# Optimization experiments

Measured on AMD Instinct MI355X. Metric: run time of the kernel, lower is better.

Reference implementation:

```python
import jax, jax.numpy as jnp
import numpy as np

DIM = 1536
HEADS = 12
HD = DIM // HEADS  # 128
EPS = 1e-6
SINK_SIZE = 1          # frames
MAX_ATTN = 1920        # tokens (sliding window)


def setup_inputs() -> dict:
    key = jax.random.key(0)
    ks = jax.random.split(key, 10)
    B = 1
    F, H, W = 8, 16, 24
    L = F * H * W  # 3072
    s = 0.02
    inp = {
        "x": jax.random.normal(ks[0], (B, L, DIM), jnp.float32),
        "seq_lens": jnp.array([L], jnp.int32),
        "grid_sizes": jnp.array([[F, H, W]], jnp.int32),
        "freqs": jax.random.normal(ks[1], (1024, HD // 2, 2), jnp.float32),
        "wq": jax.random.normal(ks[2], (DIM, DIM), jnp.float32) * s,
        "bq": jnp.zeros((DIM,), jnp.float32),
        "wk": jax.random.normal(ks[3], (DIM, DIM), jnp.float32) * s,
        "bk": jnp.zeros((DIM,), jnp.float32),
        "wv": jax.random.normal(ks[4], (DIM, DIM), jnp.float32) * s,
        "bv": jnp.zeros((DIM,), jnp.float32),
        "wo": jax.random.normal(ks[5], (DIM, DIM), jnp.float32) * s,
        "bo": jnp.zeros((DIM,), jnp.float32),
        "nq_w": jnp.ones((DIM,), jnp.float32),
        "nk_w": jnp.ones((DIM,), jnp.float32),
    }
    return inp


def _rmsnorm(x, w):
    # WanRMSNorm: x * rsqrt(mean(x^2) + eps) * weight
    return x * jax.lax.rsqrt(jnp.mean(x * x, axis=-1, keepdims=True) + EPS) * w


def _rope(x, F, H, W, fc):
    # x: [B, L, n, d]; fc: complex [1024, d//2]
    B, L, n, d = x.shape
    c = d // 2
    c1 = c - 2 * (c // 3)  # temporal split
    c2 = c // 3
    f0, f1, f2 = fc[:, :c1], fc[:, c1:c1 + c2], fc[:, c1 + c2:]
    fr = jnp.concatenate([
        jnp.broadcast_to(f0[:F, None, None, :], (F, H, W, c1)),
        jnp.broadcast_to(f1[None, :H, None, :], (F, H, W, c2)),
        jnp.broadcast_to(f2[None, None, :W, :], (F, H, W, c2)),
    ], axis=-1).reshape(L, 1, c)  # [L, 1, c]
    xp = x.reshape(B, L, n, c, 2)
    xc = jax.lax.complex(xp[..., 0], xp[..., 1])  # [B, L, n, c]
    xr = xc * fr[None]
    return jnp.stack([jnp.real(xr), jnp.imag(xr)], axis=-1).reshape(B, L, n, d)


def reference(x, seq_lens, grid_sizes, freqs, wq, bq, wk, bk, wv, bv, wo, bo, nq_w, nk_w):
    B, L, _ = x.shape
    gs = np.asarray(grid_sizes)[0]
    F, H, W = int(gs[0]), int(gs[1]), int(gs[2])
    fs = H * W  # frame_seqlen
    sink = SINK_SIZE * fs

    q = _rmsnorm(x @ wq.T + bq, nq_w).reshape(B, L, HEADS, HD)
    k = _rmsnorm(x @ wk.T + bk, nk_w).reshape(B, L, HEADS, HD)
    v = (x @ wv.T + bv).reshape(B, L, HEADS, HD)

    fc = jax.lax.complex(freqs[..., 0], freqs[..., 1])  # [1024, HD//2]
    q = _rope(q, F, H, W, fc)
    k = _rope(k, F, H, W, fc)

    # sink + windowed frame-causal block mask (flex_attention block_mask)
    idx = jnp.arange(L)
    qf = idx // fs
    kf = idx // fs
    mask = (kf[None, :] <= qf[:, None]) & (
        (idx[None, :] < sink) | (idx[None, :] >= (qf[:, None] + 1) * fs - MAX_ATTN)
    )  # [L, L]

    scale = 1.0 / np.float32(np.sqrt(HD))
    scores = jnp.einsum('bqnd,bknd->bnqk', q, k) * scale
    scores = jnp.where(mask[None, None], scores, jnp.float32(-1e30))
    attn = jax.nn.softmax(scores, axis=-1)
    out = jnp.einsum('bnqk,bknd->bqnd', attn, v).reshape(B, L, DIM)
    return out @ wo.T + bo
```

## Files before the change

### kernel.cpp

```cpp
#include <hip/hip_runtime.h>
#include <stdint.h>

#define DIMC 1536
#define LTOK 3072
#define HEADS 12
#define HD 128
#define FS 384
#define MAXATTN 1920
#define HTOK 1152
#define NHT 1920

typedef __attribute__((ext_vector_type(4))) float f32x4;
typedef __attribute__((ext_vector_type(8))) short bf16x8;
typedef __attribute__((ext_vector_type(4))) unsigned int u32x4;

__device__ __forceinline__ unsigned short f2bf(float f) {
  union { float f; unsigned int u; } c; c.f = f;
  unsigned int u = c.u + 0x7fffu + ((c.u >> 16) & 1u);
  return (unsigned short)(u >> 16);
}
__device__ __forceinline__ float bf2f(unsigned short s) {
  union { unsigned int u; float f; } c; c.u = (unsigned int)s << 16; return c.f;
}

__device__ __forceinline__ void dma16(const void* g, void* l) {
  __builtin_amdgcn_global_load_lds(
      (const __attribute__((address_space(1))) unsigned int*)g,
      (__attribute__((address_space(3))) unsigned int*)l, 16, 0, 0);
}

__global__ __launch_bounds__(256)
void cvt_all_k(const float* __restrict__ x, const float* __restrict__ wq,
               const float* __restrict__ wk, const float* __restrict__ wv,
               const float* __restrict__ wo,
               unsigned short* __restrict__ xb, unsigned short* __restrict__ wqb,
               unsigned short* __restrict__ wkb, unsigned short* __restrict__ wvb,
               unsigned short* __restrict__ wob)
{
  const int i = blockIdx.x * 256 + threadIdx.x;
  const int n0 = LTOK * DIMC / 4;
  const int nw = DIMC * DIMC / 4;
  const float* src; unsigned short* dst; int off;
  if (i < n0) { src = x; dst = xb; off = i; }
  else {
    int j = i - n0; int w = j / nw; off = j - w * nw;
    src = (w == 0) ? wq : (w == 1) ? wk : (w == 2) ? wv : wo;
    dst = (w == 0) ? wqb : (w == 1) ? wkb : (w == 2) ? wvb : wob;
  }
  float4 f = ((const float4*)src)[off];
  uint2 o;
  o.x = (unsigned int)f2bf(f.x) | ((unsigned int)f2bf(f.y) << 16);
  o.y = (unsigned int)f2bf(f.z) | ((unsigned int)f2bf(f.w) << 16);
  ((uint2*)dst)[off] = o;
}

#define GBUF (128 * 32)
__global__ __launch_bounds__(256)
void gemm_qkv(const unsigned short* __restrict__ A,
              const unsigned short* __restrict__ B0,
              const unsigned short* __restrict__ B1,
              const unsigned short* __restrict__ B2,
              const float* __restrict__ bias0,
              const float* __restrict__ bias1,
              const float* __restrict__ bias2,
              unsigned short* __restrict__ o0, unsigned short* __restrict__ o1,
              unsigned short* __restrict__ o2)
{
  const int z = blockIdx.z;
  const unsigned short* Bw = (z == 0) ? B0 : (z == 1) ? B1 : B2;
  const float* bias = (z == 0) ? bias0 : (z == 1) ? bias1 : bias2;
  unsigned short* outp = (z == 0) ? o0 : (z == 1) ? o1 : o2;

  __shared__ __align__(16) unsigned short lA[2 * GBUF];
  __shared__ __align__(16) unsigned short lB[2 * GBUF];

  const int tid = threadIdx.x;
  const int wave = tid >> 6;
  const int lane = tid & 63;
  const int m0 = blockIdx.y * 128;
  const int n0 = blockIdx.x * 128;
  const int wm = (wave >> 1) * 64;
  const int wn = (wave & 1) * 64;

  f32x4 acc[4][4] = {};

  const int srow = tid >> 2;
  const int scol = (tid & 3) * 8;
  const int fr = lane & 15;
  const int fk = (lane >> 4) * 8;

  unsigned short* laS = lA + srow * 32 + scol;
  unsigned short* lbS = lB + srow * 32 + scol;
  const unsigned short* ga0 = A  + (size_t)(m0 + srow)      * DIMC + scol;
  const unsigned short* ga1 = A  + (size_t)(m0 + srow + 64) * DIMC + scol;
  const unsigned short* gb0 = Bw + (size_t)(n0 + srow)      * DIMC + scol;
  const unsigned short* gb1 = Bw + (size_t)(n0 + srow + 64) * DIMC + scol;

  dma16(ga0, laS);
  dma16(ga1, laS + 64 * 32);
  dma16(gb0, lbS);
  dma16(gb1, lbS + 64 * 32);

  for (int t = 0; t < 48; ++t) {
    const int cur = (t & 1) * GBUF;
    __syncthreads();
    if (t < 47) {
      const int nxt = GBUF - cur;
      const int k0n = (t + 1) * 32;
      dma16(ga0 + k0n, laS + nxt);
      dma16(ga1 + k0n, laS + nxt + 64 * 32);
      dma16(gb0 + k0n, lbS + nxt);
      dma16(gb1 + k0n, lbS + nxt + 64 * 32);
    }

    bf16x8 af[4], bf[4];
#pragma unroll
    for (int i = 0; i < 4; ++i)
      af[i] = *(const bf16x8*)&lA[cur + (wm + i * 16 + fr) * 32 + fk];
#pragma unroll
    for (int j = 0; j < 4; ++j)
      bf[j] = *(const bf16x8*)&lB[cur + (wn + j * 16 + fr) * 32 + fk];
#pragma unroll
    for (int i = 0; i < 4; ++i)
#pragma unroll
      for (int j = 0; j < 4; ++j)
        acc[i][j] = __builtin_amdgcn_mfma_f32_16x16x32_bf16(af[i], bf[j], acc[i][j], 0, 0, 0);
  }

  const int col = lane & 15;
  const int rb = (lane >> 4) * 4;
#pragma unroll
  for (int j = 0; j < 4; ++j) {
    const int gn = n0 + wn + j * 16 + col;
    const float bv = bias[gn];
#pragma unroll
    for (int i = 0; i < 4; ++i)
#pragma unroll
      for (int r = 0; r < 4; ++r) {
        const int gm = m0 + wm + i * 16 + rb + r;
        outp[(size_t)gm * DIMC + gn] = f2bf(acc[i][j][r] + bv);
      }
  }
}

__global__ __launch_bounds__(512)
void gemm_wo(const unsigned short* __restrict__ A,
             const unsigned short* __restrict__ Bw,
             const float* __restrict__ bias,
             float* __restrict__ outp)
{
  __shared__ __align__(16) unsigned short lA[2 * GBUF];
  __shared__ __align__(16) unsigned short lB[2 * GBUF];

  const int tid = threadIdx.x;
  const int wave = tid >> 6;
  const int lane = tid & 63;
  const int m0 = blockIdx.y * 128;
  const int n0 = blockIdx.x * 128;
  const int wm = (wave >> 1) * 32;
  const int wn = (wave & 1) * 64;

  f32x4 acc[2][4] = {};

  const int srow = tid >> 2;
  const int scol = (tid & 3) * 8;
  const int fr = lane & 15;
  const int fk = (lane >> 4) * 8;

  unsigned short* laS = lA + srow * 32 + scol;
  unsigned short* lbS = lB + srow * 32 + scol;
  const unsigned short* ga = A  + (size_t)(m0 + srow) * DIMC + scol;
  const unsigned short* gb = Bw + (size_t)(n0 + srow) * DIMC + scol;

  dma16(ga, laS);
  dma16(gb, lbS);

  for (int t = 0; t < 48; ++t) {
    const int cur = (t & 1) * GBUF;
    __syncthreads();
    if (t < 47) {
      const int nxt = GBUF - cur;
      const int k0n = (t + 1) * 32;
      dma16(ga + k0n, laS + nxt);
      dma16(gb + k0n, lbS + nxt);
    }

    bf16x8 af[2], bf[4];
#pragma unroll
    for (int i = 0; i < 2; ++i)
      af[i] = *(const bf16x8*)&lA[cur + (wm + i * 16 + fr) * 32 + fk];
#pragma unroll
    for (int j = 0; j < 4; ++j)
      bf[j] = *(const bf16x8*)&lB[cur + (wn + j * 16 + fr) * 32 + fk];
#pragma unroll
    for (int i = 0; i < 2; ++i)
#pragma unroll
      for (int j = 0; j < 4; ++j)
        acc[i][j] = __builtin_amdgcn_mfma_f32_16x16x32_bf16(af[i], bf[j], acc[i][j], 0, 0, 0);
  }

  const int col = lane & 15;
  const int rb = (lane >> 4) * 4;
#pragma unroll
  for (int j = 0; j < 4; ++j) {
    const int gn = n0 + wn + j * 16 + col;
    const float bv = bias[gn];
#pragma unroll
    for (int i = 0; i < 2; ++i)
#pragma unroll
      for (int r = 0; r < 4; ++r) {
        const int gm = m0 + wm + i * 16 + rb + r;
        outp[(size_t)gm * DIMC + gn] = acc[i][j][r] + bv;
      }
  }
}

__device__ __forceinline__ int vperm4(int G) {
  return (((G >> 3) & 1) << 3) | (((G >> 1) & 1) << 2) | ((G & 1) << 1) | ((G >> 2) & 1);
}

__global__ __launch_bounds__(256)
void post_qkv_k(unsigned short* __restrict__ q, unsigned short* __restrict__ k,
                const unsigned short* __restrict__ v, unsigned short* __restrict__ vt,
                const float* __restrict__ nqw, const float* __restrict__ nkw,
                const float* __restrict__ freqs)
{
  const int bx = blockIdx.x;
  const int tid = threadIdx.x;
  if (bx < 2 * LTOK) {
    const int which = bx >= LTOK;
    const int tok = bx - which * LTOK;
    unsigned short* row = (which ? k : q) + (size_t)tok * DIMC;
    const float* nw = which ? nkw : nqw;
    const float sc = which ? 1.f : (0.08838834764831845f * 1.4426950408889634f);
    const int base = tid * 6;

    float vv[6];
    float ss = 0.f;
#pragma unroll
    for (int j = 0; j < 6; ++j) {
      vv[j] = bf2f(row[base + j]);
      ss += vv[j] * vv[j];
    }
#pragma unroll
    for (int off = 1; off < 64; off <<= 1) ss += __shfl_xor(ss, off);
    __shared__ float wsum[4];
    if ((tid & 63) == 0) wsum[tid >> 6] = ss;
    __syncthreads();
    const float total = wsum[0] + wsum[1] + wsum[2] + wsum[3];
    const float rms = rsqrtf(total * (1.f / DIMC) + 1e-6f);

    const int f = tok / FS;
    const int rem = tok - f * FS;
    const int h = rem / 24;
    const int w = rem - h * 24;

#pragma unroll
    for (int pp = 0; pp < 3; ++pp) {
      const int P = (base >> 1) + pp;
      const int p = P & 63;
      const int t = (p < 22) ? f : ((p < 43) ? h : w);
      const float fre = freqs[t * 128 + p * 2];
      const float fim = freqs[t * 128 + p * 2 + 1];
      const float e = vv[2 * pp]     * rms * nw[base + 2 * pp];
      const float o = vv[2 * pp + 1] * rms * nw[base + 2 * pp + 1];
      row[base + 2 * pp]     = f2bf((e * fre - o * fim) * sc);
      row[base + 2 * pp + 1] = f2bf((e * fim + o * fre) * sc);
    }
  } else {
    const int c0 = bx - 2 * LTOK;
    const int tb = (c0 % 48) * 64;
    const int db = (c0 / 48) * 64;
    __shared__ __align__(16) unsigned short t[64 * 72];
#pragma unroll
    for (int it = 0; it < 2; ++it) {
      int c = tid + it * 256;
      int tok = c >> 3, dc = (c & 7) * 8;
      uint4 val = *(const uint4*)(v + (size_t)(tb + tok) * DIMC + db + dc);
      unsigned short tmp[8];
      *(uint4*)tmp = val;
#pragma unroll
      for (int j = 0; j < 8; ++j) t[(dc + j) * 72 + tok] = tmp[j];
    }
    __syncthreads();
#pragma unroll
    for (int it = 0; it < 4; ++it) {
      int c = tid + it * 256;
      int d = c >> 4, G = c & 15;
      *(uint2*)(vt + ((size_t)db + d) * LTOK + tb + vperm4(G) * 4) =
          *(const uint2*)&t[d * 72 + G * 4];
    }
  }
}

#define KBUF (64 * 128)
#define VBUF (128 * 64)
__global__ __launch_bounds__(256, 2)
void attn_flash(const unsigned short* __restrict__ q,
                const unsigned short* __restrict__ k,
                const unsigned short* __restrict__ vt,
                unsigned short* __restrict__ ab,
                float* __restrict__ Opart,
                float* __restrict__ mlbuf)
{
  const int bid = blockIdx.x;
  int qb, head, chunk, nchunks;
  if (bid < 360) { const int hb = bid >> 1; qb = 23 - hb / 12; head = hb % 12; chunk = bid & 1; nchunks = 2; }
  else           { const int lb = bid - 360; qb = 8 - lb / 12; head = lb % 12; chunk = 0; nchunks = 1; }

  const int q0 = qb * 128;
  const int qf = qb / 3;
  const int kend = (qf + 1) * FS;
  const int s2 = kend - MAXATTN;
  const bool two = (s2 > FS);
  const int nt1 = (two ? FS : kend) >> 6;
  const int nt  = nt1 + (two ? (MAXATTN >> 6) : 0);
  const int half = nt / nchunks;
  const int tstart = chunk * half, tend = tstart + half;

  const int tid = threadIdx.x;
  const int wave = tid >> 6, lane = tid & 63;
  const int col = lane & 15;
  const int g = lane >> 4;
  const int g4 = g * 4;

  __shared__ __align__(16) unsigned short Kl[2 * KBUF];
  __shared__ __align__(16) unsigned short Vtl[2 * VBUF];

  bf16x8 qfA[4], qfB[4];
  {
    const unsigned short* qr0 = q + (size_t)(q0 + wave * 32 + col) * DIMC + head * HD;
#pragma unroll
    for (int kk = 0; kk < 4; ++kk) {
      qfA[kk] = *(const bf16x8*)(qr0 + kk * 32 + g * 8);
      qfB[kk] = *(const bf16x8*)(qr0 + (size_t)16 * DIMC + kk * 32 + g * 8);
    }
  }

  f32x4 o0[8] = {}, o1[8] = {};
  float m0 = -3.0e38f, l0 = 0.f, m1 = -3.0e38f, l1 = 0.f;

  const int krow = tid >> 4;
  const int kc8  = ((tid & 15) ^ krow) * 8;
  const unsigned short* kg = k + (size_t)krow * DIMC + head * HD + kc8;
  const int vrow = tid >> 3;
  const int vc8  = ((tid & 7) ^ (vrow & 7)) * 8;
  const unsigned short* vg = vt + ((size_t)head * HD + vrow) * LTOK + vc8;
  unsigned short* kl = Kl + tid * 8;
  unsigned short* vl = Vtl + tid * 8;

  {
    const int kb = (tstart < nt1) ? tstart * 64 : s2 + (tstart - nt1) * 64;
    const unsigned short* kp = kg + (size_t)kb * DIMC;
    dma16(kp,                     kl);
    dma16(kp + (size_t)16 * DIMC, kl + 16 * 128);
    dma16(kp + (size_t)32 * DIMC, kl + 32 * 128);
    dma16(kp + (size_t)48 * DIMC, kl + 48 * 128);
    const unsigned short* vp = vg + kb;
    dma16(vp,                     vl);
    dma16(vp + (size_t)32 * LTOK, vl + 32 * 64);
    dma16(vp + (size_t)64 * LTOK, vl + 64 * 64);
    dma16(vp + (size_t)96 * LTOK, vl + 96 * 64);
  }

  for (int t = tstart; t < tend; ++t) {
    const int kcur = ((t - tstart) & 1) * KBUF;
    const int vcur = ((t - tstart) & 1) * VBUF;
    __syncthreads();

    if (t + 1 < tend) {
      const int kb = (t + 1 < nt1) ? (t + 1) * 64 : s2 + (t + 1 - nt1) * 64;
      const int knxt = KBUF - kcur, vnxt = VBUF - vcur;
      const unsigned short* kp = kg + (size_t)kb * DIMC;
      dma16(kp,                     kl + knxt);
      dma16(kp + (size_t)16 * DIMC, kl + knxt + 16 * 128);
      dma16(kp + (size_t)32 * DIMC, kl + knxt + 32 * 128);
      dma16(kp + (size_t)48 * DIMC, kl + knxt + 48 * 128);
      const unsigned short* vp = vg + kb;
      dma16(vp,                     vl + vnxt);
      dma16(vp + (size_t)32 * LTOK, vl + vnxt + 32 * 64);
      dma16(vp + (size_t)64 * LTOK, vl + vnxt + 64 * 64);
      dma16(vp + (size_t)96 * LTOK, vl + vnxt + 96 * 64);
    }

    f32x4 sA[4] = {}, sB[4] = {};
#pragma unroll
    for (int kt = 0; kt < 4; ++kt) {
      const unsigned short* kr = &Kl[kcur + (kt * 16 + col) * 128];
#pragma unroll
      for (int kk = 0; kk < 4; ++kk) {
        bf16x8 kfr = *(const bf16x8*)(kr + ((kk * 4 + g) ^ col) * 8);
        sA[kt] = __builtin_amdgcn_mfma_f32_16x16x32_bf16(kfr, qfA[kk], sA[kt], 0, 0, 0);
        sB[kt] = __builtin_amdgcn_mfma_f32_16x16x32_bf16(kfr, qfB[kk], sB[kt], 0, 0, 0);
      }
    }

    unsigned int A0, A1, A2, A3, A4, A5, A6, A7;
    float alA;
    {
      float mx = sA[0][0];
#pragma unroll
      for (int kt = 0; kt < 4; ++kt)
#pragma unroll
        for (int r = 0; r < 4; ++r) mx = fmaxf(mx, sA[kt][r]);
      mx = fmaxf(mx, __shfl_xor(mx, 16));
      mx = fmaxf(mx, __shfl_xor(mx, 32));
      const float mn = fmaxf(m0, mx);
      alA = exp2f(m0 - mn);
      m0 = mn;
      float rs = 0.f;
#define PKA(KT, PA, PB)                                        \
      {                                                        \
        const unsigned short p0 = f2bf(exp2f(sA[KT][0] - mn)); \
        const unsigned short p1 = f2bf(exp2f(sA[KT][1] - mn)); \
        const unsigned short p2 = f2bf(exp2f(sA[KT][2] - mn)); \
        const unsigned short p3 = f2bf(exp2f(sA[KT][3] - mn)); \
        rs += bf2f(p0) + bf2f(p1) + bf2f(p2) + bf2f(p3);       \
        PA = (unsigned int)p0 | ((unsigned int)p1 << 16);      \
        PB = (unsigned int)p2 | ((unsigned int)p3 << 16);      \
      }
      PKA(0, A0, A1) PKA(1, A2, A3) PKA(2, A4, A5) PKA(3, A6, A7)
#undef PKA
      rs += __shfl_xor(rs, 16);
      rs += __shfl_xor(rs, 32);
      l0 = l0 * alA + rs;
    }
    unsigned int B0, B1, B2, B3, B4, B5, B6, B7;
    float alB;
    {
      float mx = sB[0][0];
#pragma unroll
      for (int kt = 0; kt < 4; ++kt)
#pragma unroll
        for (int r = 0; r < 4; ++r) mx = fmaxf(mx, sB[kt][r]);
      mx = fmaxf(mx, __shfl_xor(mx, 16));
      mx = fmaxf(mx, __shfl_xor(mx, 32));
      const float mn = fmaxf(m1, mx);
      alB = exp2f(m1 - mn);
      m1 = mn;
      float rs = 0.f;
#define PKB(KT, PA, PB)                                        \
      {                                                        \
        const unsigned short p0 = f2bf(exp2f(sB[KT][0] - mn)); \
        const unsigned short p1 = f2bf(exp2f(sB[KT][1] - mn)); \
        const unsigned short p2 = f2bf(exp2f(sB[KT][2] - mn)); \
        const unsigned short p3 = f2bf(exp2f(sB[KT][3] - mn)); \
        rs += bf2f(p0) + bf2f(p1) + bf2f(p2) + bf2f(p3);       \
        PA = (unsigned int)p0 | ((unsigned int)p1 << 16);      \
        PB = (unsigned int)p2 | ((unsigned int)p3 << 16);      \
      }
      PKB(0, B0, B1) PKB(1, B2, B3) PKB(2, B4, B5) PKB(3, B6, B7)
#undef PKB
      rs += __shfl_xor(rs, 16);
      rs += __shfl_xor(rs, 32);
      l1 = l1 * alB + rs;
    }

#pragma unroll
    for (int dt = 0; dt < 8; ++dt) { o0[dt] *= alA; o1[dt] *= alB; }

    u32x4 tA0, tA1, tB0, tB1;
    tA0[0] = A0; tA0[1] = A1; tA0[2] = A2; tA0[3] = A3;
    tA1[0] = A4; tA1[1] = A5; tA1[2] = A6; tA1[3] = A7;
    tB0[0] = B0; tB0[1] = B1; tB0[2] = B2; tB0[3] = B3;
    tB1[0] = B4; tB1[1] = B5; tB1[2] = B6; tB1[3] = B7;
    const bf16x8 pfA0 = __builtin_bit_cast(bf16x8, tA0);
    const bf16x8 pfA1 = __builtin_bit_cast(bf16x8, tA1);
    const bf16x8 pfB0 = __builtin_bit_cast(bf16x8, tB0);
    const bf16x8 pfB1 = __builtin_bit_cast(bf16x8, tB1);

    const int vx0 = (g ^ (col & 7)) * 8;
    const int vx1 = ((4 + g) ^ (col & 7)) * 8;
#pragma unroll
    for (int dt = 0; dt < 8; ++dt) {
      const unsigned short* vr = &Vtl[vcur + (dt * 16 + col) * 64];
      bf16x8 vf0 = *(const bf16x8*)(vr + vx0);
      o0[dt] = __builtin_amdgcn_mfma_f32_16x16x32_bf16(vf0, pfA0, o0[dt], 0, 0, 0);
      o1[dt] = __builtin_amdgcn_mfma_f32_16x16x32_bf16(vf0, pfB0, o1[dt], 0, 0, 0);
      bf16x8 vf1 = *(const bf16x8*)(vr + vx1);
      o0[dt] = __builtin_amdgcn_mfma_f32_16x16x32_bf16(vf1, pfA1, o0[dt], 0, 0, 0);
      o1[dt] = __builtin_amdgcn_mfma_f32_16x16x32_bf16(vf1, pfB1, o1[dt], 0, 0, 0);
    }
  }

  const int qrow0 = q0 + wave * 32 + col;
  if (nchunks == 1) {
    const float i0 = 1.f / l0, i1 = 1.f / l1;
    unsigned short* or0 = ab + (size_t)qrow0 * DIMC + head * HD;
    unsigned short* or1 = or0 + (size_t)16 * DIMC;
#pragma unroll
    for (int dt = 0; dt < 8; ++dt) {
      uint2 pk;
      pk.x = (unsigned int)f2bf(o0[dt][0] * i0) | ((unsigned int)f2bf(o0[dt][1] * i0) << 16);
      pk.y = (unsigned int)f2bf(o0[dt][2] * i0) | ((unsigned int)f2bf(o0[dt][3] * i0) << 16);
      *(uint2*)(or0 + dt * 16 + g4) = pk;
      pk.x = (unsigned int)f2bf(o1[dt][0] * i1) | ((unsigned int)f2bf(o1[dt][1] * i1) << 16);
      pk.y = (unsigned int)f2bf(o1[dt][2] * i1) | ((unsigned int)f2bf(o1[dt][3] * i1) << 16);
      *(uint2*)(or1 + dt * 16 + g4) = pk;
    }
  } else {
    const int tokp0 = qrow0 - HTOK;
    float* ob0 = Opart + ((size_t)(chunk * NHT + tokp0) * HEADS + head) * HD;
    float* ob1 = Opart + ((size_t)(chunk * NHT + tokp0 + 16) * HEADS + head) * HD;
#pragma unroll
    for (int dt = 0; dt < 8; ++dt) {
      *(f32x4*)(ob0 + dt * 16 + g4) = o0[dt];
      *(f32x4*)(ob1 + dt * 16 + g4) = o1[dt];
    }
    if (lane < 16) {
      float* mlp0 = mlbuf + 2 * ((size_t)(chunk * NHT + tokp0) * HEADS + head);
      float* mlp1 = mlbuf + 2 * ((size_t)(chunk * NHT + tokp0 + 16) * HEADS + head);
      mlp0[0] = m0; mlp0[1] = l0;
      mlp1[0] = m1; mlp1[1] = l1;
    }
  }
}

__global__ __launch_bounds__(384)
void merge_k(const float* __restrict__ Opart, const float* __restrict__ mlbuf,
             unsigned short* __restrict__ ab)
{
  const int tokp = blockIdx.x;
  const int tid = threadIdx.x;
  const int e = tid * 4;
  const int head = e >> 7;
  const size_t r0 = (size_t)tokp * DIMC + e;
  float4 o0 = *(const float4*)(Opart + r0);
  float4 o1 = *(const float4*)(Opart + (size_t)NHT * DIMC + r0);
  const float* ml0 = mlbuf + 2 * ((size_t)tokp * HEADS + head);
  const float* ml1 = mlbuf + 2 * ((size_t)(NHT + tokp) * HEADS + head);
  const float m0 = ml0[0], l0 = ml0[1], m1 = ml1[0], l1 = ml1[1];
  const float mm = fmaxf(m0, m1);
  const float a0 = exp2f(m0 - mm), a1 = exp2f(m1 - mm);
  const float inv = 1.f / (l0 * a0 + l1 * a1);
  uint2 pk;
  pk.x = (unsigned int)f2bf((o0.x * a0 + o1.x * a1) * inv) |
         ((unsigned int)f2bf((o0.y * a0 + o1.y * a1) * inv) << 16);
  pk.y = (unsigned int)f2bf((o0.z * a0 + o1.z * a1) * inv) |
         ((unsigned int)f2bf((o0.w * a0 + o1.w * a1) * inv) << 16);
  *(uint2*)(ab + (size_t)(HTOK + tokp) * DIMC + e) = pk;
}

extern "C" void kernel_launch(void* const* d_in, const int* in_sizes, int n_in,
                              void* d_out, int out_size, void* d_ws, size_t ws_size,
                              hipStream_t stream)
{
  (void)in_sizes; (void)n_in; (void)out_size; (void)ws_size;
  const float* x     = (const float*)d_in[0];
  const float* freqs = (const float*)d_in[3];
  const float* wq    = (const float*)d_in[4];
  const float* bq    = (const float*)d_in[5];
  const float* wk    = (const float*)d_in[6];
  const float* bk    = (const float*)d_in[7];
  const float* wv    = (const float*)d_in[8];
  const float* bv    = (const float*)d_in[9];
  const float* wo    = (const float*)d_in[10];
  const float* bo    = (const float*)d_in[11];
  const float* nqw   = (const float*)d_in[12];
  const float* nkw   = (const float*)d_in[13];

  char* ws = (char*)d_ws;
  size_t off = 0;
  auto take = [&](size_t bytes) -> void* {
    void* p = ws + off; off += (bytes + 255) & ~(size_t)255; return p;
  };
  unsigned short* wob = (unsigned short*)take((size_t)DIMC * DIMC * 2);
  unsigned short* qb  = (unsigned short*)take((size_t)LTOK * DIMC * 2);
  unsigned short* kb  = (unsigned short*)take((size_t)LTOK * DIMC * 2);
  unsigned short* vb  = (unsigned short*)take((size_t)LTOK * DIMC * 2);
  unsigned short* ab  = (unsigned short*)take((size_t)LTOK * DIMC * 2);
  unsigned short* vtb = (unsigned short*)take((size_t)LTOK * DIMC * 2);
  unsigned short* xb  = (unsigned short*)take((size_t)LTOK * DIMC * 2);
  unsigned short* wqb = (unsigned short*)take((size_t)DIMC * DIMC * 2);
  unsigned short* wkb = (unsigned short*)take((size_t)DIMC * DIMC * 2);
  unsigned short* wvb = (unsigned short*)take((size_t)DIMC * DIMC * 2);
  float* mlb = (float*)take((size_t)2 * NHT * HEADS * 2 * sizeof(float));
  float* Opart = (float*)xb;

  cvt_all_k<<<dim3(13824), dim3(256), 0, stream>>>(x, wq, wk, wv, wo,
                                                   xb, wqb, wkb, wvb, wob);

  gemm_qkv<<<dim3(DIMC / 128, LTOK / 128, 3), dim3(256), 0, stream>>>(
      xb, wqb, wkb, wvb, bq, bk, bv, qb, kb, vb);

  post_qkv_k<<<dim3(2 * LTOK + 1152), dim3(256), 0, stream>>>(
      qb, kb, vb, vtb, nqw, nkw, freqs);

  attn_flash<<<dim3(468), dim3(256), 0, stream>>>(qb, kb, vtb, ab, Opart, mlb);
  merge_k<<<dim3(NHT), dim3(384), 0, stream>>>(Opart, mlb, ab);

  gemm_wo<<<dim3(DIMC / 128, LTOK / 128), dim3(512), 0, stream>>>(
      ab, wob, bo, (float*)d_out);
}
```

Baseline: 318.5 us.

## Fuse V transpose into QKV GEMM epilogue and retile GEMMs with swizzled K=64 LDS

The QKV GEMM now writes V directly in the transposed, permuted layout the attention kernel reads, which removes the separate transpose blocks from post_qkv_k and one round trip of V through memory. Both GEMMs move from double-buffered K=32 stages to single-buffered K=64 stages with an XOR-swizzled LDS layout meant to reduce bank conflicts. gemm_wo also changes from 512-thread 128x128 tiles to 256-thread 64x128 tiles. Dropping double buffering means global loads are no longer overlapped with MFMA work, which could expose load latency, and the transposed V stores are 8-byte scattered writes.

```diff
diff --git a/kernel.cpp b/kernel.cpp
--- a/kernel.cpp
+++ b/kernel.cpp
@@ -27,6 +27,10 @@
   __builtin_amdgcn_global_load_lds(
       (const __attribute__((address_space(1))) unsigned int*)g,
       (__attribute__((address_space(3))) unsigned int*)l, 16, 0, 0);
+}
+
+__device__ __forceinline__ int vperm4(int G) {
+  return (((G >> 3) & 1) << 3) | (((G >> 1) & 1) << 2) | ((G & 1) << 1) | ((G >> 2) & 1);
 }
 
 __global__ __launch_bounds__(256)
@@ -54,7 +58,6 @@
   ((uint2*)dst)[off] = o;
 }
 
-#define GBUF (128 * 32)
 __global__ __launch_bounds__(256)
 void gemm_qkv(const unsigned short* __restrict__ A,
               const unsigned short* __restrict__ B0,
@@ -64,15 +67,14 @@
               const float* __restrict__ bias1,
               const float* __restrict__ bias2,
               unsigned short* __restrict__ o0, unsigned short* __restrict__ o1,
-              unsigned short* __restrict__ o2)
+              unsigned short* __restrict__ vt)
 {
   const int z = blockIdx.z;
   const unsigned short* Bw = (z == 0) ? B0 : (z == 1) ? B1 : B2;
   const float* bias = (z == 0) ? bias0 : (z == 1) ? bias1 : bias2;
-  unsigned short* outp = (z == 0) ? o0 : (z == 1) ? o1 : o2;
-
-  __shared__ __align__(16) unsigned short lA[2 * GBUF];
-  __shared__ __align__(16) unsigned short lB[2 * GBUF];
+
+  __shared__ __align__(16) unsigned short lA[128 * 64];
+  __shared__ __align__(16) unsigned short lB[128 * 64];
 
   const int tid = threadIdx.x;
   const int wave = tid >> 6;
@@ -84,119 +86,140 @@
 
   f32x4 acc[4][4] = {};
 
-  const int srow = tid >> 2;
-  const int scol = (tid & 3) * 8;
+  const int srow = tid >> 3;
+  const int scol = ((tid & 7) ^ (srow & 7)) * 8;
+  const unsigned short* ga = A  + (size_t)(m0 + srow) * DIMC + scol;
+  const unsigned short* gb = Bw + (size_t)(n0 + srow) * DIMC + scol;
+  unsigned short* la = lA + tid * 8;
+  unsigned short* lb = lB + tid * 8;
+
   const int fr = lane & 15;
-  const int fk = (lane >> 4) * 8;
-
-  unsigned short* laS = lA + srow * 32 + scol;
-  unsigned short* lbS = lB + srow * 32 + scol;
-  const unsigned short* ga0 = A  + (size_t)(m0 + srow)      * DIMC + scol;
-  const unsigned short* ga1 = A  + (size_t)(m0 + srow + 64) * DIMC + scol;
-  const unsigned short* gb0 = Bw + (size_t)(n0 + srow)      * DIMC + scol;
-  const unsigned short* gb1 = Bw + (size_t)(n0 + srow + 64) * DIMC + scol;
-
-  dma16(ga0, laS);
-  dma16(ga1, laS + 64 * 32);
-  dma16(gb0, lbS);
-  dma16(gb1, lbS + 64 * 32);
-
-  for (int t = 0; t < 48; ++t) {
-    const int cur = (t & 1) * GBUF;
+  const int g = lane >> 4;
+  const int fx = fr & 7;
+
+  for (int k0 = 0; k0 < DIMC; k0 += 64) {
+    dma16(ga + k0,                     la);
+    dma16(ga + k0 + (size_t)32 * DIMC, la + 2048);
+    dma16(ga + k0 + (size_t)64 * DIMC, la + 4096);
+    dma16(ga + k0 + (size_t)96 * DIMC, la + 6144);
+    dma16(gb + k0,                     lb);
+    dma16(gb + k0 + (size_t)32 * DIMC, lb + 2048);
+    dma16(gb + k0 + (size_t)64 * DIMC, lb + 4096);
+    dma16(gb + k0 + (size_t)96 * DIMC, lb + 6144);
     __syncthreads();
-    if (t < 47) {
-      const int nxt = GBUF - cur;
-      const int k0n = (t + 1) * 32;
-      dma16(ga0 + k0n, laS + nxt);
-      dma16(ga1 + k0n, laS + nxt + 64 * 32);
-      dma16(gb0 + k0n, lbS + nxt);
-      dma16(gb1 + k0n, lbS + nxt + 64 * 32);
-    }
-
-    bf16x8 af[4], bf[4];
-#pragma unroll
-    for (int i = 0; i < 4; ++i)
-      af[i] = *(const bf16x8*)&lA[cur + (wm + i * 16 + fr) * 32 + fk];
-#pragma unroll
-    for (int j = 0; j < 4; ++j)
-      bf[j] = *(const bf16x8*)&lB[cur + (wn + j * 16 + fr) * 32 + fk];
-#pragma unroll
-    for (int i = 0; i < 4; ++i)
+
+#pragma unroll
+    for (int kk = 0; kk < 2; ++kk) {
+      const int cx = ((kk * 4 + g) ^ fx) * 8;
+      bf16x8 af[4], bf[4];
+#pragma unroll
+      for (int i = 0; i < 4; ++i)
+        af[i] = *(const bf16x8*)&lA[(wm + i * 16 + fr) * 64 + cx];
 #pragma unroll
       for (int j = 0; j < 4; ++j)
-        acc[i][j] = __builtin_amdgcn_mfma_f32_16x16x32_bf16(af[i], bf[j], acc[i][j], 0, 0, 0);
+        bf[j] = *(const bf16x8*)&lB[(wn + j * 16 + fr) * 64 + cx];
+#pragma unroll
+      for (int i = 0; i < 4; ++i)
+#pragma unroll
+        for (int j = 0; j < 4; ++j)
+          acc[i][j] = __builtin_amdgcn_mfma_f32_16x16x32_bf16(af[i], bf[j], acc[i][j], 0, 0, 0);
+    }
+    __syncthreads();
   }
 
   const int col = lane & 15;
   const int rb = (lane >> 4) * 4;
-#pragma unroll
-  for (int j = 0; j < 4; ++j) {
-    const int gn = n0 + wn + j * 16 + col;
-    const float bv = bias[gn];
-#pragma unroll
-    for (int i = 0; i < 4; ++i)
-#pragma unroll
-      for (int r = 0; r < 4; ++r) {
-        const int gm = m0 + wm + i * 16 + rb + r;
-        outp[(size_t)gm * DIMC + gn] = f2bf(acc[i][j][r] + bv);
+  if (z < 2) {
+    unsigned short* outp = z ? o1 : o0;
+#pragma unroll
+    for (int j = 0; j < 4; ++j) {
+      const int gn = n0 + wn + j * 16 + col;
+      const float bv = bias[gn];
+#pragma unroll
+      for (int i = 0; i < 4; ++i)
+#pragma unroll
+        for (int r = 0; r < 4; ++r) {
+          const int gm = m0 + wm + i * 16 + rb + r;
+          outp[(size_t)gm * DIMC + gn] = f2bf(acc[i][j][r] + bv);
+        }
+    }
+  } else {
+#pragma unroll
+    for (int j = 0; j < 4; ++j) {
+      const int gn = n0 + wn + j * 16 + col;
+      const float bv = bias[gn];
+#pragma unroll
+      for (int i = 0; i < 4; ++i) {
+        const int base = wm + i * 16 + rb;
+        const int tile = base & ~63;
+        const int toka = m0 + tile + vperm4((base & 63) >> 2) * 4;
+        uint2 pk;
+        pk.x = (unsigned int)f2bf(acc[i][j][0] + bv) |
+               ((unsigned int)f2bf(acc[i][j][1] + bv) << 16);
+        pk.y = (unsigned int)f2bf(acc[i][j][2] + bv) |
+               ((unsigned int)f2bf(acc[i][j][3] + bv) << 16);
+        *(uint2*)(vt + (size_t)gn * LTOK + toka) = pk;
       }
-  }
-}
-
-__global__ __launch_bounds__(512)
+    }
+  }
+}
+
+__global__ __launch_bounds__(256)
 void gemm_wo(const unsigned short* __restrict__ A,
              const unsigned short* __restrict__ Bw,
              const float* __restrict__ bias,
              float* __restrict__ outp)
 {
-  __shared__ __align__(16) unsigned short lA[2 * GBUF];
-  __shared__ __align__(16) unsigned short lB[2 * GBUF];
+  __shared__ __align__(16) unsigned short lA[64 * 64];
+  __shared__ __align__(16) unsigned short lB[128 * 64];
 
   const int tid = threadIdx.x;
   const int wave = tid >> 6;
   const int lane = tid & 63;
-  const int m0 = blockIdx.y * 128;
+  const int m0 = blockIdx.y * 64;
   const int n0 = blockIdx.x * 128;
   const int wm = (wave >> 1) * 32;
   const int wn = (wave & 1) * 64;
 
   f32x4 acc[2][4] = {};
 
-  const int srow = tid >> 2;
-  const int scol = (tid & 3) * 8;
-  const int fr = lane & 15;
-  const int fk = (lane >> 4) * 8;
-
-  unsigned short* laS = lA + srow * 32 + scol;
-  unsigned short* lbS = lB + srow * 32 + scol;
+  const int srow = tid >> 3;
+  const int scol = ((tid & 7) ^ (srow & 7)) * 8;
   const unsigned short* ga = A  + (size_t)(m0 + srow) * DIMC + scol;
   const unsigned short* gb = Bw + (size_t)(n0 + srow) * DIMC + scol;
-
-  dma16(ga, laS);
-  dma16(gb, lbS);
-
-  for (int t = 0; t < 48; ++t) {
-    const int cur = (t & 1) * GBUF;
+  unsigned short* la = lA + tid * 8;
+  unsigned short* lb = lB + tid * 8;
+
+  const int fr = lane & 15;
+  const int g = lane >> 4;
+  const int fx = fr & 7;
+
+  for (int k0 = 0; k0 < DIMC; k0 += 64) {
+    dma16(ga + k0,                     la);
+    dma16(ga + k0 + (size_t)32 * DIMC, la + 2048);
+    dma16(gb + k0,                     lb);
+    dma16(gb + k0 + (size_t)32 * DIMC, lb + 2048);
+    dma16(gb + k0 + (size_t)64 * DIMC, lb + 4096);
+    dma16(gb + k0 + (size_t)96 * DIMC, lb + 6144);
     __syncthreads();
-    if (t < 47) {
-      const int nxt = GBUF - cur;
-      const int k0n = (t + 1) * 32;
-      dma16(ga + k0n, laS + nxt);
-      dma16(gb + k0n, lbS + nxt);
-    }
-
-    bf16x8 af[2], bf[4];
-#pragma unroll
-    for (int i = 0; i < 2; ++i)
-      af[i] = *(const bf16x8*)&lA[cur + (wm + i * 16 + fr) * 32 + fk];
-#pragma unroll
-    for (int j = 0; j < 4; ++j)
-      bf[j] = *(const bf16x8*)&lB[cur + (wn + j * 16 + fr) * 32 + fk];
-#pragma unroll
-    for (int i = 0; i < 2; ++i)
+
+#pragma unroll
+    for (int kk = 0; kk < 2; ++kk) {
+      const int cx = ((kk * 4 + g) ^ fx) * 8;
+      bf16x8 af[2], bf[4];
+#pragma unroll
+      for (int i = 0; i < 2; ++i)
+        af[i] = *(const bf16x8*)&lA[(wm + i * 16 + fr) * 64 + cx];
 #pragma unroll
       for (int j = 0; j < 4; ++j)
-        acc[i][j] = __builtin_amdgcn_mfma_f32_16x16x32_bf16(af[i], bf[j], acc[i][j], 0, 0, 0);
+        bf[j] = *(const bf16x8*)&lB[(wn + j * 16 + fr) * 64 + cx];
+#pragma unroll
+      for (int i = 0; i < 2; ++i)
+#pragma unroll
+        for (int j = 0; j < 4; ++j)
+          acc[i][j] = __builtin_amdgcn_mfma_f32_16x16x32_bf16(af[i], bf[j], acc[i][j], 0, 0, 0);
+    }
+    __syncthreads();
   }
 
   const int col = lane & 15;
@@ -215,81 +238,51 @@
   }
 }
 
-__device__ __forceinline__ int vperm4(int G) {
-  return (((G >> 3) & 1) << 3) | (((G >> 1) & 1) << 2) | ((G & 1) << 1) | ((G >> 2) & 1);
-}
-
 __global__ __launch_bounds__(256)
 void post_qkv_k(unsigned short* __restrict__ q, unsigned short* __restrict__ k,
-                const unsigned short* __restrict__ v, unsigned short* __restrict__ vt,
                 const float* __restrict__ nqw, const float* __restrict__ nkw,
                 const float* __restrict__ freqs)
 {
   const int bx = blockIdx.x;
   const int tid = threadIdx.x;
-  if (bx < 2 * LTOK) {
-    const int which = bx >= LTOK;
-    const int tok = bx - which * LTOK;
-    unsigned short* row = (which ? k : q) + (size_t)tok * DIMC;
-    const float* nw = which ? nkw : nqw;
-    const float sc = which ? 1.f : (0.08838834764831845f * 1.4426950408889634f);
-    const int base = tid * 6;
-
-    float vv[6];
-    float ss = 0.f;
-#pragma unroll
-    for (int j = 0; j < 6; ++j) {
-      vv[j] = bf2f(row[base + j]);
-      ss += vv[j] * vv[j];
-    }
-#pragma unroll
-    for (int off = 1; off < 64; off <<= 1) ss += __shfl_xor(ss, off);
-    __shared__ float wsum[4];
-    if ((tid & 63) == 0) wsum[tid >> 6] = ss;
-    __syncthreads();
-    const float total = wsum[0] + wsum[1] + wsum[2] + wsum[3];
-    const float rms = rsqrtf(total * (1.f / DIMC) + 1e-6f);
-
-    const int f = tok / FS;
-    const int rem = tok - f * FS;
-    const int h = rem / 24;
-    const int w = rem - h * 24;
-
-#pragma unroll
-    for (int pp = 0; pp < 3; ++pp) {
-      const int P = (base >> 1) + pp;
-      const int p = P & 63;
-      const int t = (p < 22) ? f : ((p < 43) ? h : w);
-      const float fre = freqs[t * 128 + p * 2];
-      const float fim = freqs[t * 128 + p * 2 + 1];
-      const float e = vv[2 * pp]     * rms * nw[base + 2 * pp];
-      const float o = vv[2 * pp + 1] * rms * nw[base + 2 * pp + 1];
-      row[base + 2 * pp]     = f2bf((e * fre - o * fim) * sc);
-      row[base + 2 * pp + 1] = f2bf((e * fim + o * fre) * sc);
-    }
-  } else {
-    const int c0 = bx - 2 * LTOK;
-    const int tb = (c0 % 48) * 64;
-    const int db = (c0 / 48) * 64;
-    __shared__ __align__(16) unsigned short t[64 * 72];
-#pragma unroll
-    for (int it = 0; it < 2; ++it) {
-      int c = tid + it * 256;
-      int tok = c >> 3, dc = (c & 7) * 8;
-      uint4 val = *(const uint4*)(v + (size_t)(tb + tok) * DIMC + db + dc);
-      unsigned short tmp[8];
-      *(uint4*)tmp = val;
-#pragma unroll
-      for (int j = 0; j < 8; ++j) t[(dc + j) * 72 + tok] = tmp[j];
-    }
-    __syncthreads();
-#pragma unroll
-    for (int it = 0; it < 4; ++it) {
-      int c = tid + it * 256;
-      int d = c >> 4, G = c & 15;
-      *(uint2*)(vt + ((size_t)db + d) * LTOK + tb + vperm4(G) * 4) =
-          *(const uint2*)&t[d * 72 + G * 4];
-    }
+  const int which = bx >= LTOK;
+  const int tok = bx - which * LTOK;
+  unsigned short* row = (which ? k : q) + (size_t)tok * DIMC;
+  const float* nw = which ? nkw : nqw;
+  const float sc = which ? 1.f : (0.08838834764831845f * 1.4426950408889634f);
+  const int base = tid * 6;
+
+  float vv[6];
+  float ss = 0.f;
+#pragma unroll
+  for (int j = 0; j < 6; ++j) {
+    vv[j] = bf2f(row[base + j]);
+    ss += vv[j] * vv[j];
+  }
+#pragma unroll
+  for (int off = 1; off < 64; off <<= 1) ss += __shfl_xor(ss, off);
+  __shared__ float wsum[4];
+  if ((tid & 63) == 0) wsum[tid >> 6] = ss;
+  __syncthreads();
+  const float total = wsum[0] + wsum[1] + wsum[2] + wsum[3];
+  const float rms = rsqrtf(total * (1.f / DIMC) + 1e-6f);
+
+  const int f = tok / FS;
+  const int rem = tok - f * FS;
+  const int h = rem / 24;
+  const int w = rem - h * 24;
+
+#pragma unroll
+  for (int pp = 0; pp < 3; ++pp) {
+    const int P = (base >> 1) + pp;
+    const int p = P & 63;
+    const int t = (p < 22) ? f : ((p < 43) ? h : w);
+    const float fre = freqs[t * 128 + p * 2];
+    const float fim = freqs[t * 128 + p * 2 + 1];
+    const float e = vv[2 * pp]     * rms * nw[base + 2 * pp];
+    const float o = vv[2 * pp + 1] * rms * nw[base + 2 * pp + 1];
+    row[base + 2 * pp]     = f2bf((e * fre - o * fim) * sc);
+    row[base + 2 * pp + 1] = f2bf((e * fim + o * fre) * sc);
   }
 }
 
@@ -576,19 +569,19 @@
   unsigned short* wvb = (unsigned short*)take((size_t)DIMC * DIMC * 2);
   float* mlb = (float*)take((size_t)2 * NHT * HEADS * 2 * sizeof(float));
   float* Opart = (float*)xb;
+  (void)vb;
 
   cvt_all_k<<<dim3(13824), dim3(256), 0, stream>>>(x, wq, wk, wv, wo,
                                                    xb, wqb, wkb, wvb, wob);
 
   gemm_qkv<<<dim3(DIMC / 128, LTOK / 128, 3), dim3(256), 0, stream>>>(
-      xb, wqb, wkb, wvb, bq, bk, bv, qb, kb, vb);
-
-  post_qkv_k<<<dim3(2 * LTOK + 1152), dim3(256), 0, stream>>>(
-      qb, kb, vb, vtb, nqw, nkw, freqs);
+      xb, wqb, wkb, wvb, bq, bk, bv, qb, kb, vtb);
+
+  post_qkv_k<<<dim3(2 * LTOK), dim3(256), 0, stream>>>(qb, kb, nqw, nkw, freqs);
 
   attn_flash<<<dim3(468), dim3(256), 0, stream>>>(qb, kb, vtb, ab, Opart, mlb);
   merge_k<<<dim3(NHT), dim3(384), 0, stream>>>(Opart, mlb, ab);
 
-  gemm_wo<<<dim3(DIMC / 128, LTOK / 128), dim3(512), 0, stream>>>(
+  gemm_wo<<<dim3(DIMC / 128, LTOK / 64), dim3(256), 0, stream>>>(
       ab, wob, bo, (float*)d_out);
 }
```

Measured after the change: 285.0 us. -10.5%, faster.
